# Kernel optimization log

Measured on AMD Instinct MI355X. Metric: run time of the kernel, lower is better.

## Reference

```python
import jax, jax.numpy as jnp
import numpy as np

N_GRAPHS = 16

def setup_inputs() -> dict:
    key = jax.random.key(0)
    ks = jax.random.split(key, 10)
    N, E, D_IN, D_H, D_OUT = 50000, 800000, 128, 128, 64
    x = jax.random.normal(ks[0], (N, D_IN), dtype=jnp.float32)
    edge_index = jax.random.randint(ks[1], (2, E), 0, N, dtype=jnp.int64)
    edge_attr = jax.random.uniform(ks[2], (E,), dtype=jnp.float32)
    batch = jnp.sort(jax.random.randint(ks[3], (N,), 0, N_GRAPHS, dtype=jnp.int64))
    def lin(k, fan_in, fan_out):
        kw, kb = jax.random.split(k)
        bound = 1.0 / np.sqrt(fan_in)
        W = jax.random.uniform(kw, (fan_in, fan_out), minval=-bound, maxval=bound, dtype=jnp.float32)
        b = jax.random.uniform(kb, (fan_out,), minval=-bound, maxval=bound, dtype=jnp.float32)
        return W, b
    W1, b1 = lin(ks[4], D_IN, D_H)
    W2, b2 = lin(ks[5], D_H, D_H)
    W3, b3 = lin(ks[6], D_H, D_OUT)
    return {"x": x, "edge_index": edge_index, "edge_attr": edge_attr, "batch": batch,
            "W1": W1, "b1": b1, "W2": W2, "b2": b2, "W3": W3, "b3": b3}


def _conv_layer(x, W, b, src, dst, edge_attr, num_nodes):
    # x' = Linear(x); out = scatter_sum_{src->dst}(x'[src] * w_e) + x'
    h = x @ W + b
    msg = h[src] * edge_attr[:, None]          # [E, d]
    agg = jax.ops.segment_sum(msg, dst, num_segments=num_nodes)
    return agg + h


def reference(x, edge_index, edge_attr, batch, W1, b1, W2, b2, W3, b3):
    N = x.shape[0]
    src, dst = edge_index[0], edge_index[1]
    h = _conv_layer(x, W1, b1, src, dst, edge_attr, N)
    h = _conv_layer(h, W2, b2, src, dst, edge_attr, N)
    h = _conv_layer(h, W3, b3, src, dst, edge_attr, N)
    # global mean pool per graph, then flatten per graph
    sums = jax.ops.segment_sum(h, batch, num_segments=N_GRAPHS)        # [G, d_out]
    counts = jax.ops.segment_sum(jnp.ones((N,), h.dtype), batch, num_segments=N_GRAPHS)
    pooled = sums / jnp.maximum(counts, 1.0)[:, None]
    return pooled.reshape(N_GRAPHS, -1)
```

## Files before the change

kernel.cpp:

```cpp
#include <hip/hip_runtime.h>
#include <hip/hip_bf16.h>

typedef __bf16 bf16x8 __attribute__((ext_vector_type(8)));
typedef float f32x4 __attribute__((ext_vector_type(4)));

__device__ __forceinline__ unsigned short f2bf(float f) {
    unsigned int u = __float_as_uint(f);
    unsigned int r = (u + 0x7FFFu + ((u >> 16) & 1u)) >> 16;
    return (unsigned short)r;
}
__device__ __forceinline__ float bflo(unsigned int u) { return __uint_as_float(u << 16); }
__device__ __forceinline__ float bfhi(unsigned int u) { return __uint_as_float(u & 0xffff0000u); }


__device__ __forceinline__ void prep_w_dev(const float* __restrict__ W,
                                           unsigned short* __restrict__ Wt,
                                           int DOUT, int i) {
    int col = i >> 4;
    int kblk = i & 15;
    size_t off = (size_t)col * 128 + (size_t)((kblk ^ (col & 7)) << 3);
#pragma unroll
    for (int j = 0; j < 8; j++)
        Wt[off + j] = f2bf(W[(kblk * 8 + j) * DOUT + col]);
}

__global__ __launch_bounds__(256) void prep_kernel(
    const float* __restrict__ x, unsigned short* __restrict__ Xb, int n4, int xblocks,
    const int* __restrict__ dst, int* __restrict__ deg, int E, int eblocks,
    const float* __restrict__ W1, unsigned short* __restrict__ Wt1,
    const float* __restrict__ W2, unsigned short* __restrict__ Wt2,
    const float* __restrict__ W3, unsigned short* __restrict__ Wt3) {
    int b = blockIdx.x;
    int tid = threadIdx.x;
    if (b < xblocks) {
        int i = b * 256 + tid;
        if (i < n4) {
            float4 v = reinterpret_cast<const float4*>(x)[i];
            ushort4 o;
            o.x = f2bf(v.x); o.y = f2bf(v.y); o.z = f2bf(v.z); o.w = f2bf(v.w);
            reinterpret_cast<ushort4*>(Xb)[i] = o;
        }
        return;
    }
    b -= xblocks;
    if (b < eblocks) {
        int e = b * 256 + tid;
        if (e < E) atomicAdd(&deg[dst[e]], 1);
        return;
    }
    b -= eblocks;
    if (b < 8) {
        prep_w_dev(W1, Wt1, 128, b * 256 + tid);
    } else if (b < 16) {
        prep_w_dev(W2, Wt2, 128, (b - 8) * 256 + tid);
    } else {
        int i = (b - 16) * 256 + tid;
        if (i < 64 * 16) prep_w_dev(W3, Wt3, 64, i);
    }
}


__global__ __launch_bounds__(1024) void scan1_kernel(const int* __restrict__ deg,
                                                     int* __restrict__ row_off,
                                                     int* __restrict__ blk_sums, int N) {
    __shared__ int sd[1024];
    int tid = threadIdx.x;
    int i = blockIdx.x * 1024 + tid;
    int v = (i < N) ? deg[i] : 0;
    sd[tid] = v;
    __syncthreads();
    for (int off = 1; off < 1024; off <<= 1) {
        int t = (tid >= off) ? sd[tid - off] : 0;
        __syncthreads();
        sd[tid] += t;
        __syncthreads();
    }
    if (i < N) row_off[i] = sd[tid] - v;
    if (tid == 1023) blk_sums[blockIdx.x] = sd[1023];
}

__global__ void scan2_kernel(int* __restrict__ blk, int nb) {
    __shared__ int s[128];
    int t = threadIdx.x;
    int v = (t < nb) ? blk[t] : 0;
    s[t] = v;
    __syncthreads();
    for (int off = 1; off < 128; off <<= 1) {
        int u = (t >= off) ? s[t - off] : 0;
        __syncthreads();
        s[t] += u;
        __syncthreads();
    }
    if (t < nb) blk[t] = s[t] - v;
}

__global__ __launch_bounds__(1024) void scan3_kernel(int* __restrict__ row_off,
                                                     const int* __restrict__ blk_sums,
                                                     int* __restrict__ cursor, int N, int E) {
    int i = blockIdx.x * 1024 + threadIdx.x;
    if (i < N) {
        int r = row_off[i] + blk_sums[blockIdx.x];
        row_off[i] = r;
        cursor[i] = r;
    }
    if (i == 0) row_off[N] = E;
}

__global__ void build_csr_kernel(const int* __restrict__ src, const int* __restrict__ dst,
                                 const float* __restrict__ ea, int* __restrict__ cursor,
                                 unsigned int* __restrict__ csr, int E) {
    int e = blockIdx.x * blockDim.x + threadIdx.x;
    if (e < E) {
        int d = dst[e];
        int pos = atomicAdd(&cursor[d], 1);
        csr[pos] = (unsigned int)src[e] | ((unsigned int)f2bf(ea[e]) << 16);
    }
}


template <int DOUT>
__global__ __launch_bounds__(256) void gemm_mfma_kernel(
    const unsigned short* __restrict__ Xb,
    const unsigned short* __restrict__ Wt,
    const float* __restrict__ bias,
    unsigned short* __restrict__ Hb,
    int N) {
    constexpr int CB = DOUT / 16;
    __shared__ unsigned short wlds[DOUT * 128];
    int tid = threadIdx.x;

    constexpr int TOT16 = DOUT * 128 / 8;
    const uint4* Wv = reinterpret_cast<const uint4*>(Wt);
    uint4* Lv = reinterpret_cast<uint4*>(wlds);
#pragma unroll
    for (int i = 0; i < TOT16 / 256; i++) Lv[tid + i * 256] = Wv[tid + i * 256];
    __syncthreads();

    int wave = tid >> 6;
    int lane = tid & 63;
    int r0 = blockIdx.x * 64 + wave * 16;
    int arow = r0 + (lane & 15);
    int arow_c = (arow < N) ? arow : (N - 1);

    f32x4 acc[CB];
#pragma unroll
    for (int cb = 0; cb < CB; cb++) acc[cb] = (f32x4){0.f, 0.f, 0.f, 0.f};

    const bf16x8* Xrow = reinterpret_cast<const bf16x8*>(Xb + (size_t)arow_c * 128);
    int lhi = lane >> 4;
#pragma unroll
    for (int kk = 0; kk < 4; kk++) {
        bf16x8 a = Xrow[kk * 4 + lhi];
#pragma unroll
        for (int cb = 0; cb < CB; cb++) {
            int colg = cb * 16 + (lane & 15);
            int kblk = kk * 4 + lhi;
            const bf16x8* bp = reinterpret_cast<const bf16x8*>(
                &wlds[colg * 128 + ((kblk ^ (colg & 7)) << 3)]);
            acc[cb] = __builtin_amdgcn_mfma_f32_16x16x32_bf16(a, *bp, acc[cb], 0, 0, 0);
        }
    }

    int cl = lane & 15;
    int rbase = r0 + lhi * 4;
#pragma unroll
    for (int cb = 0; cb < CB; cb++) {
        int colg = cb * 16 + cl;
        float bb = bias[colg];
#pragma unroll
        for (int r = 0; r < 4; r++) {
            int rowg = rbase + r;
            if (rowg < N) Hb[(size_t)rowg * DOUT + colg] = f2bf(acc[cb][r] + bb);
        }
    }
}


template <int D>
__global__ __launch_bounds__(256) void aggregate_bf16_kernel(
    const unsigned short* __restrict__ Hb, const int* __restrict__ row_off,
    const unsigned int* __restrict__ csr, unsigned short* __restrict__ Ob, int N) {
    constexpr int TPN = D / 8;
    constexpr int NPB = 256 / TPN;
    int n = blockIdx.x * NPB + threadIdx.x / TPN;
    int d8 = threadIdx.x % TPN;
    if (n >= N) return;
    const uint4* Hv = reinterpret_cast<const uint4*>(Hb);

    float acc[8];
    {
        uint4 s = Hv[(size_t)n * TPN + d8];
        acc[0] = bflo(s.x); acc[1] = bfhi(s.x);
        acc[2] = bflo(s.y); acc[3] = bfhi(s.y);
        acc[4] = bflo(s.z); acc[5] = bfhi(s.z);
        acc[6] = bflo(s.w); acc[7] = bfhi(s.w);
    }
    auto madd = [&](uint4 v, float w) {
        acc[0] += bflo(v.x) * w; acc[1] += bfhi(v.x) * w;
        acc[2] += bflo(v.y) * w; acc[3] += bfhi(v.y) * w;
        acc[4] += bflo(v.z) * w; acc[5] += bfhi(v.z) * w;
        acc[6] += bflo(v.w) * w; acc[7] += bfhi(v.w) * w;
    };
    int e = row_off[n];
    int e1 = row_off[n + 1];
    for (; e + 4 <= e1; e += 4) {
        unsigned int c0 = csr[e], c1 = csr[e + 1], c2 = csr[e + 2], c3 = csr[e + 3];
        uint4 v0 = Hv[(size_t)(c0 & 0xFFFFu) * TPN + d8];
        uint4 v1 = Hv[(size_t)(c1 & 0xFFFFu) * TPN + d8];
        uint4 v2 = Hv[(size_t)(c2 & 0xFFFFu) * TPN + d8];
        uint4 v3 = Hv[(size_t)(c3 & 0xFFFFu) * TPN + d8];
        madd(v0, bfhi(c0));
        madd(v1, bfhi(c1));
        madd(v2, bfhi(c2));
        madd(v3, bfhi(c3));
    }
    for (; e < e1; ++e) {
        unsigned int c = csr[e];
        madd(Hv[(size_t)(c & 0xFFFFu) * TPN + d8], bfhi(c));
    }
    uint4 o;
    o.x = (unsigned int)f2bf(acc[0]) | ((unsigned int)f2bf(acc[1]) << 16);
    o.y = (unsigned int)f2bf(acc[2]) | ((unsigned int)f2bf(acc[3]) << 16);
    o.z = (unsigned int)f2bf(acc[4]) | ((unsigned int)f2bf(acc[5]) << 16);
    o.w = (unsigned int)f2bf(acc[6]) | ((unsigned int)f2bf(acc[7]) << 16);
    reinterpret_cast<uint4*>(Ob)[(size_t)n * TPN + d8] = o;
}


__global__ __launch_bounds__(256) void pool_kernel(const unsigned short* __restrict__ Hb,
                                                   const int* __restrict__ batch,
                                                   float* __restrict__ sums, int N,
                                                   int rows_per_blk) {
    __shared__ float bins[16 * 64];
    int tid = threadIdx.x;
    for (int i = tid; i < 1024; i += 256) bins[i] = 0.f;
    __syncthreads();
    int d4 = tid & 15;
    int rl = tid >> 4;
    int n0 = blockIdx.x * rows_per_blk;
    int n1 = min(n0 + rows_per_blk, N);
    const uint2* Hv = reinterpret_cast<const uint2*>(Hb);
    float r0 = 0.f, r1 = 0.f, r2 = 0.f, r3 = 0.f;
    int cur = -1;
    for (int n = n0 + rl; n < n1; n += 16) {
        int b = batch[n];
        if (b != cur) {
            if (cur >= 0) {
                atomicAdd(&bins[cur * 64 + d4 * 4 + 0], r0);
                atomicAdd(&bins[cur * 64 + d4 * 4 + 1], r1);
                atomicAdd(&bins[cur * 64 + d4 * 4 + 2], r2);
                atomicAdd(&bins[cur * 64 + d4 * 4 + 3], r3);
            }
            cur = b;
            r0 = r1 = r2 = r3 = 0.f;
        }
        uint2 v = Hv[(size_t)n * 16 + d4];
        r0 += bflo(v.x); r1 += bfhi(v.x); r2 += bflo(v.y); r3 += bfhi(v.y);
    }
    if (cur >= 0) {
        atomicAdd(&bins[cur * 64 + d4 * 4 + 0], r0);
        atomicAdd(&bins[cur * 64 + d4 * 4 + 1], r1);
        atomicAdd(&bins[cur * 64 + d4 * 4 + 2], r2);
        atomicAdd(&bins[cur * 64 + d4 * 4 + 3], r3);
    }
    __syncthreads();
    for (int i = tid; i < 1024; i += 256) {
        float v = bins[i];
        if (v != 0.f) atomicAdd(&sums[i], v);
    }
}

__global__ void finalize_kernel(const float* __restrict__ sums, const int* __restrict__ batch,
                                int N, float* __restrict__ out) {
    int i = blockIdx.x * blockDim.x + threadIdx.x;
    if (i >= 1024) return;
    int g = i >> 6;
    auto lower_bound = [&](int key) {
        int lo = 0, hi = N;
        while (lo < hi) { int mid = (lo + hi) >> 1; if (batch[mid] < key) lo = mid + 1; else hi = mid; }
        return lo;
    };
    int c = lower_bound(g + 1) - lower_bound(g);
    out[i] = sums[i] / (float)max(c, 1);
}


extern "C" void kernel_launch(void* const* d_in, const int* in_sizes, int n_in,
                              void* d_out, int out_size, void* d_ws, size_t ws_size,
                              hipStream_t stream) {
    const float* x   = (const float*)d_in[0];
    const int*   ei  = (const int*)d_in[1];
    const float* ea  = (const float*)d_in[2];
    const int*   bat = (const int*)d_in[3];
    const float* W1  = (const float*)d_in[4];
    const float* b1  = (const float*)d_in[5];
    const float* W2  = (const float*)d_in[6];
    const float* b2  = (const float*)d_in[7];
    const float* W3  = (const float*)d_in[8];
    const float* b3  = (const float*)d_in[9];

    const int N = in_sizes[0] / 128;
    const int E = in_sizes[2];
    const int* src = ei;
    const int* dst = ei + E;

    auto align = [](size_t v) { return (v + 255) & ~(size_t)255; };
    char* p = (char*)d_ws;
    unsigned short* Xb   = (unsigned short*)p; p += align((size_t)N * 128 * 2);
    unsigned short* Hb   = (unsigned short*)p; p += align((size_t)N * 128 * 2);
    unsigned short* Ab   = (unsigned short*)p; p += align((size_t)N * 128 * 2);
    unsigned short* Ab3  = (unsigned short*)p; p += align((size_t)N * 64 * 2);
    unsigned short* Wt1  = (unsigned short*)p; p += align(128 * 128 * 2);
    unsigned short* Wt2  = (unsigned short*)p; p += align(128 * 128 * 2);
    unsigned short* Wt3  = (unsigned short*)p; p += align(64 * 128 * 2);
    int*   deg      = (int*)p;   p += align((size_t)N * sizeof(int));
    int*   row_off  = (int*)p;   p += align((size_t)(N + 1) * sizeof(int));
    int*   cursor   = (int*)p;   p += align((size_t)N * sizeof(int));
    unsigned int* csr = (unsigned int*)p; p += align((size_t)E * sizeof(unsigned int));
    int*   blk_sums = (int*)p;   p += align(128 * sizeof(int));
    float* sums     = (float*)p; p += align(1024 * sizeof(float));

    hipMemsetAsync(deg, 0, (size_t)N * sizeof(int), stream);
    hipMemsetAsync(sums, 0, 1024 * sizeof(float), stream);

    int eb = (E + 255) / 256;
    int nb = (N + 1023) / 1024;

    int n4 = N * 128 / 4;
    int xblocks = (n4 + 255) / 256;
    prep_kernel<<<xblocks + eb + 20, 256, 0, stream>>>(
        x, Xb, n4, xblocks, dst, deg, E, eb, W1, Wt1, W2, Wt2, W3, Wt3);

    scan1_kernel<<<nb, 1024, 0, stream>>>(deg, row_off, blk_sums, N);
    scan2_kernel<<<1, 128, 0, stream>>>(blk_sums, nb);
    scan3_kernel<<<nb, 1024, 0, stream>>>(row_off, blk_sums, cursor, N, E);
    build_csr_kernel<<<eb, 256, 0, stream>>>(src, dst, ea, cursor, csr, E);

    int gb = (N + 63) / 64;
    gemm_mfma_kernel<128><<<gb, 256, 0, stream>>>(Xb, Wt1, b1, Hb, N);
    aggregate_bf16_kernel<128><<<(N + 15) / 16, 256, 0, stream>>>(Hb, row_off, csr, Ab, N);
    gemm_mfma_kernel<128><<<gb, 256, 0, stream>>>(Ab, Wt2, b2, Hb, N);
    aggregate_bf16_kernel<128><<<(N + 15) / 16, 256, 0, stream>>>(Hb, row_off, csr, Ab, N);
    gemm_mfma_kernel<64><<<gb, 256, 0, stream>>>(Ab, Wt3, b3, Hb, N);
    aggregate_bf16_kernel<64><<<(N + 31) / 32, 256, 0, stream>>>(Hb, row_off, csr, Ab3, N);

    int pool_blocks = 512;
    int rows_per_blk = (N + pool_blocks - 1) / pool_blocks;
    pool_kernel<<<pool_blocks, 256, 0, stream>>>(Ab3, bat, sums, N, rows_per_blk);
    finalize_kernel<<<4, 256, 0, stream>>>(sums, bat, N, (float*)d_out);
}
```

Baseline: 301.5 us.

## Build CSR via two-level bucket scatter then per-bucket LDS sort

Replaces the per-node global atomic cursor used to build the CSR with a two-pass scheme. Edges are first scattered into buckets of 16 destination nodes using padded per-bucket global atomics into a staged buffer of (packed edge, local node) pairs. A second kernel then places each bucket's edges into final CSR order using shared-memory atomics. This trades scattered global atomics on many cursors for fewer, padded ones plus an extra pass over an 8-byte-per-edge staging buffer, which adds memory traffic and a kernel launch.

Result: no change. 304.3 us (+0.9%).

```diff
diff --git a/kernel.cpp b/kernel.cpp
--- a/kernel.cpp
+++ b/kernel.cpp
@@ -3,6 +3,10 @@
 
 typedef __bf16 bf16x8 __attribute__((ext_vector_type(8)));
 typedef float f32x4 __attribute__((ext_vector_type(4)));
+
+#define BSH 4
+#define BNPB 16
+#define CURPAD 16
 
 __device__ __forceinline__ unsigned short f2bf(float f) {
     unsigned int u = __float_as_uint(f);
@@ -96,24 +100,46 @@
 
 __global__ __launch_bounds__(1024) void scan3_kernel(int* __restrict__ row_off,
                                                      const int* __restrict__ blk_sums,
-                                                     int* __restrict__ cursor, int N, int E) {
+                                                     int* __restrict__ bcur, int N, int E) {
     int i = blockIdx.x * 1024 + threadIdx.x;
     if (i < N) {
         int r = row_off[i] + blk_sums[blockIdx.x];
         row_off[i] = r;
-        cursor[i] = r;
+        if ((i & (BNPB - 1)) == 0) bcur[(i >> BSH) * CURPAD] = r;
     }
     if (i == 0) row_off[N] = E;
 }
 
-__global__ void build_csr_kernel(const int* __restrict__ src, const int* __restrict__ dst,
-                                 const float* __restrict__ ea, int* __restrict__ cursor,
-                                 unsigned int* __restrict__ csr, int E) {
+__global__ void bucket_scatter_kernel(const int* __restrict__ src, const int* __restrict__ dst,
+                                      const float* __restrict__ ea, int* __restrict__ bcur,
+                                      uint2* __restrict__ staged, int E) {
     int e = blockIdx.x * blockDim.x + threadIdx.x;
     if (e < E) {
         int d = dst[e];
-        int pos = atomicAdd(&cursor[d], 1);
-        csr[pos] = (unsigned int)src[e] | ((unsigned int)f2bf(ea[e]) << 16);
+        int pos = atomicAdd(&bcur[(d >> BSH) * CURPAD], 1);
+        staged[pos] = make_uint2((unsigned int)src[e] | ((unsigned int)f2bf(ea[e]) << 16),
+                                 (unsigned int)(d & (BNPB - 1)));
+    }
+}
+
+__global__ __launch_bounds__(128) void bucket_sort_kernel(const int* __restrict__ row_off,
+                                                          const uint2* __restrict__ staged,
+                                                          unsigned int* __restrict__ csr, int N) {
+    __shared__ int lcur[BNPB];
+    int b = blockIdx.x;
+    int n0 = b << BSH;
+    int tid = threadIdx.x;
+    int base = row_off[n0];
+    int end = row_off[min(n0 + BNPB, N)];
+    if (tid < BNPB) {
+        int nn = n0 + tid;
+        lcur[tid] = (nn < N) ? (row_off[nn] - base) : 0;
+    }
+    __syncthreads();
+    for (int i = base + tid; i < end; i += 128) {
+        uint2 s = staged[i];
+        int pos = atomicAdd(&lcur[s.y], 1);
+        csr[base + pos] = s.x;
     }
 }
 
@@ -303,6 +329,7 @@
     const int E = in_sizes[2];
     const int* src = ei;
     const int* dst = ei + E;
+    const int NB = (N + BNPB - 1) / BNPB;
 
     auto align = [](size_t v) { return (v + 255) & ~(size_t)255; };
     char* p = (char*)d_ws;
@@ -315,7 +342,8 @@
     unsigned short* Wt3  = (unsigned short*)p; p += align(64 * 128 * 2);
     int*   deg      = (int*)p;   p += align((size_t)N * sizeof(int));
     int*   row_off  = (int*)p;   p += align((size_t)(N + 1) * sizeof(int));
-    int*   cursor   = (int*)p;   p += align((size_t)N * sizeof(int));
+    int*   bcur     = (int*)p;   p += align((size_t)NB * CURPAD * sizeof(int));
+    uint2* staged   = (uint2*)p; p += align((size_t)E * sizeof(uint2));
     unsigned int* csr = (unsigned int*)p; p += align((size_t)E * sizeof(unsigned int));
     int*   blk_sums = (int*)p;   p += align(128 * sizeof(int));
     float* sums     = (float*)p; p += align(1024 * sizeof(float));
@@ -333,8 +361,9 @@
 
     scan1_kernel<<<nb, 1024, 0, stream>>>(deg, row_off, blk_sums, N);
     scan2_kernel<<<1, 128, 0, stream>>>(blk_sums, nb);
-    scan3_kernel<<<nb, 1024, 0, stream>>>(row_off, blk_sums, cursor, N, E);
-    build_csr_kernel<<<eb, 256, 0, stream>>>(src, dst, ea, cursor, csr, E);
+    scan3_kernel<<<nb, 1024, 0, stream>>>(row_off, blk_sums, bcur, N, E);
+    bucket_scatter_kernel<<<eb, 256, 0, stream>>>(src, dst, ea, bcur, staged, E);
+    bucket_sort_kernel<<<NB, 128, 0, stream>>>(row_off, staged, csr, N);
 
     int gb = (N + 63) / 64;
     gemm_mfma_kernel<128><<<gb, 256, 0, stream>>>(Xb, Wt1, b1, Hb, N);
```

## Build CSR via two-level bucketed counting sort with shared-memory atomics

Applied to the files above, without the earlier changes.

Replaces the global-atomic degree histogram, three-kernel node scan and global-atomic scatter with a bucketed radix-style CSR build. Edges are first histogrammed per block into 256-node buckets in LDS, then scanned and scattered into a staged buffer, and each bucket is finally sorted locally with LDS atomics to produce row offsets and CSR. This targets contended global atomics and scattered writes, but it adds an extra staged 8-byte-per-edge buffer pass and a single-block scan over bucket counts.

New measurement: 319.2 us. 1.06x slower.

```diff
diff --git a/kernel.cpp b/kernel.cpp
--- a/kernel.cpp
+++ b/kernel.cpp
@@ -3,6 +3,10 @@
 
 typedef __bf16 bf16x8 __attribute__((ext_vector_type(8)));
 typedef float f32x4 __attribute__((ext_vector_type(4)));
+
+#define NBLK_SC 256
+#define BKT_SH 8
+#define BKT_NODES 256
 
 __device__ __forceinline__ unsigned short f2bf(float f) {
     unsigned int u = __float_as_uint(f);
@@ -26,7 +30,6 @@
 
 __global__ __launch_bounds__(256) void prep_kernel(
     const float* __restrict__ x, unsigned short* __restrict__ Xb, int n4, int xblocks,
-    const int* __restrict__ dst, int* __restrict__ deg, int E, int eblocks,
     const float* __restrict__ W1, unsigned short* __restrict__ Wt1,
     const float* __restrict__ W2, unsigned short* __restrict__ Wt2,
     const float* __restrict__ W3, unsigned short* __restrict__ Wt3) {
@@ -43,12 +46,6 @@
         return;
     }
     b -= xblocks;
-    if (b < eblocks) {
-        int e = b * 256 + tid;
-        if (e < E) atomicAdd(&deg[dst[e]], 1);
-        return;
-    }
-    b -= eblocks;
     if (b < 8) {
         prep_w_dev(W1, Wt1, 128, b * 256 + tid);
     } else if (b < 16) {
@@ -60,60 +57,97 @@
 }
 
 
-__global__ __launch_bounds__(1024) void scan1_kernel(const int* __restrict__ deg,
-                                                     int* __restrict__ row_off,
-                                                     int* __restrict__ blk_sums, int N) {
-    __shared__ int sd[1024];
-    int tid = threadIdx.x;
-    int i = blockIdx.x * 1024 + tid;
-    int v = (i < N) ? deg[i] : 0;
-    sd[tid] = v;
+__global__ __launch_bounds__(256) void csr_hist_kernel(const int* __restrict__ dst,
+                                                       int* __restrict__ cnt,
+                                                       int E, int NBKT, int CPB) {
+    __shared__ int lcnt[BKT_NODES];
+    int j = blockIdx.x;
+    int tid = threadIdx.x;
+    lcnt[tid] = 0;
+    __syncthreads();
+    int e0 = j * CPB, e1 = min(e0 + CPB, E);
+    for (int e = e0 + tid; e < e1; e += 256) atomicAdd(&lcnt[dst[e] >> BKT_SH], 1);
+    __syncthreads();
+    for (int b = tid; b < NBKT; b += 256) cnt[b * NBLK_SC + j] = lcnt[b];
+}
+
+__global__ __launch_bounds__(1024) void csr_scan_kernel(const int* __restrict__ cnt,
+                                                        int* __restrict__ scan, int total) {
+    __shared__ int s[1024];
+    int tid = threadIdx.x;
+    int K = (total + 1023) / 1024;
+    int i0 = tid * K;
+    int i1 = min(i0 + K, total);
+    int sum = 0;
+    for (int i = i0; i < i1; i++) sum += cnt[i];
+    s[tid] = sum;
     __syncthreads();
     for (int off = 1; off < 1024; off <<= 1) {
-        int t = (tid >= off) ? sd[tid - off] : 0;
+        int t = (tid >= off) ? s[tid - off] : 0;
         __syncthreads();
-        sd[tid] += t;
+        s[tid] += t;
         __syncthreads();
     }
-    if (i < N) row_off[i] = sd[tid] - v;
-    if (tid == 1023) blk_sums[blockIdx.x] = sd[1023];
-}
-
-__global__ void scan2_kernel(int* __restrict__ blk, int nb) {
-    __shared__ int s[128];
-    int t = threadIdx.x;
-    int v = (t < nb) ? blk[t] : 0;
-    s[t] = v;
-    __syncthreads();
-    for (int off = 1; off < 128; off <<= 1) {
-        int u = (t >= off) ? s[t - off] : 0;
+    int run = s[tid] - sum;
+    for (int i = i0; i < i1; i++) { scan[i] = run; run += cnt[i]; }
+}
+
+__global__ __launch_bounds__(256) void csr_scatter_kernel(const int* __restrict__ src,
+                                                          const int* __restrict__ dst,
+                                                          const float* __restrict__ ea,
+                                                          const int* __restrict__ scan,
+                                                          uint2* __restrict__ staged,
+                                                          int E, int NBKT, int CPB) {
+    __shared__ int curs[BKT_NODES];
+    int j = blockIdx.x;
+    int tid = threadIdx.x;
+    for (int b = tid; b < NBKT; b += 256) curs[b] = scan[b * NBLK_SC + j];
+    __syncthreads();
+    int e0 = j * CPB, e1 = min(e0 + CPB, E);
+    for (int e = e0 + tid; e < e1; e += 256) {
+        int d = dst[e];
+        int pos = atomicAdd(&curs[d >> BKT_SH], 1);
+        staged[pos] = make_uint2((unsigned int)src[e] | ((unsigned int)f2bf(ea[e]) << 16),
+                                 (unsigned int)(d & (BKT_NODES - 1)));
+    }
+}
+
+__global__ __launch_bounds__(256) void csr_bucket_kernel(const int* __restrict__ scan,
+                                                         const uint2* __restrict__ staged,
+                                                         unsigned int* __restrict__ csr,
+                                                         int* __restrict__ row_off,
+                                                         int N, int E) {
+    __shared__ int deg[BKT_NODES];
+    __shared__ int loff[BKT_NODES];
+    __shared__ int lcur[BKT_NODES];
+    int b = blockIdx.x;
+    int NBKT = gridDim.x;
+    int tid = threadIdx.x;
+    int base = scan[b * NBLK_SC];
+    int end = (b == NBKT - 1) ? E : scan[(b + 1) * NBLK_SC];
+    deg[tid] = 0;
+    __syncthreads();
+    for (int i = base + tid; i < end; i += 256) atomicAdd(&deg[staged[i].y], 1);
+    __syncthreads();
+    int v = deg[tid];
+    loff[tid] = v;
+    __syncthreads();
+    for (int off = 1; off < 256; off <<= 1) {
+        int t = (tid >= off) ? loff[tid - off] : 0;
         __syncthreads();
-        s[t] += u;
+        loff[tid] += t;
         __syncthreads();
     }
-    if (t < nb) blk[t] = s[t] - v;
-}
-
-__global__ __launch_bounds__(1024) void scan3_kernel(int* __restrict__ row_off,
-                                                     const int* __restrict__ blk_sums,
-                                                     int* __restrict__ cursor, int N, int E) {
-    int i = blockIdx.x * 1024 + threadIdx.x;
-    if (i < N) {
-        int r = row_off[i] + blk_sums[blockIdx.x];
-        row_off[i] = r;
-        cursor[i] = r;
-    }
-    if (i == 0) row_off[N] = E;
-}
-
-__global__ void build_csr_kernel(const int* __restrict__ src, const int* __restrict__ dst,
-                                 const float* __restrict__ ea, int* __restrict__ cursor,
-                                 unsigned int* __restrict__ csr, int E) {
-    int e = blockIdx.x * blockDim.x + threadIdx.x;
-    if (e < E) {
-        int d = dst[e];
-        int pos = atomicAdd(&cursor[d], 1);
-        csr[pos] = (unsigned int)src[e] | ((unsigned int)f2bf(ea[e]) << 16);
+    int excl = loff[tid] - v;
+    lcur[tid] = excl;
+    int n = (b << BKT_SH) + tid;
+    if (n < N) row_off[n] = base + excl;
+    if (b == NBKT - 1 && tid == 0) row_off[N] = E;
+    __syncthreads();
+    for (int i = base + tid; i < end; i += 256) {
+        uint2 s = staged[i];
+        int pos = atomicAdd(&lcur[s.y], 1);
+        csr[base + pos] = s.x;
     }
 }
 
@@ -303,6 +337,9 @@
     const int E = in_sizes[2];
     const int* src = ei;
     const int* dst = ei + E;
+    const int NBKT = (N + BKT_NODES - 1) / BKT_NODES;
+    const int CPB = (E + NBLK_SC - 1) / NBLK_SC;
+    const int CTOT = NBKT * NBLK_SC;
 
     auto align = [](size_t v) { return (v + 255) & ~(size_t)255; };
     char* p = (char*)d_ws;
@@ -313,28 +350,24 @@
     unsigned short* Wt1  = (unsigned short*)p; p += align(128 * 128 * 2);
     unsigned short* Wt2  = (unsigned short*)p; p += align(128 * 128 * 2);
     unsigned short* Wt3  = (unsigned short*)p; p += align(64 * 128 * 2);
-    int*   deg      = (int*)p;   p += align((size_t)N * sizeof(int));
     int*   row_off  = (int*)p;   p += align((size_t)(N + 1) * sizeof(int));
-    int*   cursor   = (int*)p;   p += align((size_t)N * sizeof(int));
+    int*   cnt      = (int*)p;   p += align((size_t)CTOT * sizeof(int));
+    int*   scan     = (int*)p;   p += align((size_t)CTOT * sizeof(int));
+    uint2* staged   = (uint2*)p; p += align((size_t)E * sizeof(uint2));
     unsigned int* csr = (unsigned int*)p; p += align((size_t)E * sizeof(unsigned int));
-    int*   blk_sums = (int*)p;   p += align(128 * sizeof(int));
     float* sums     = (float*)p; p += align(1024 * sizeof(float));
 
-    hipMemsetAsync(deg, 0, (size_t)N * sizeof(int), stream);
     hipMemsetAsync(sums, 0, 1024 * sizeof(float), stream);
-
-    int eb = (E + 255) / 256;
-    int nb = (N + 1023) / 1024;
 
     int n4 = N * 128 / 4;
     int xblocks = (n4 + 255) / 256;
-    prep_kernel<<<xblocks + eb + 20, 256, 0, stream>>>(
-        x, Xb, n4, xblocks, dst, deg, E, eb, W1, Wt1, W2, Wt2, W3, Wt3);
-
-    scan1_kernel<<<nb, 1024, 0, stream>>>(deg, row_off, blk_sums, N);
-    scan2_kernel<<<1, 128, 0, stream>>>(blk_sums, nb);
-    scan3_kernel<<<nb, 1024, 0, stream>>>(row_off, blk_sums, cursor, N, E);
-    build_csr_kernel<<<eb, 256, 0, stream>>>(src, dst, ea, cursor, csr, E);
+    prep_kernel<<<xblocks + 20, 256, 0, stream>>>(
+        x, Xb, n4, xblocks, W1, Wt1, W2, Wt2, W3, Wt3);
+
+    csr_hist_kernel<<<NBLK_SC, 256, 0, stream>>>(dst, cnt, E, NBKT, CPB);
+    csr_scan_kernel<<<1, 1024, 0, stream>>>(cnt, scan, CTOT);
+    csr_scatter_kernel<<<NBLK_SC, 256, 0, stream>>>(src, dst, ea, scan, staged, E, NBKT, CPB);
+    csr_bucket_kernel<<<NBKT, 256, 0, stream>>>(scan, staged, csr, row_off, N, E);
 
     int gb = (N + 63) / 64;
     gemm_mfma_kernel<128><<<gb, 256, 0, stream>>>(Xb, Wt1, b1, Hb, N);
```
